# Optimization experiments

Hardware: AMD Instinct MI355X
Metric: run time of the kernel (lower is better)

The kernel has to match this reference:

```python
import jax, jax.numpy as jnp
import numpy as np

IN_DIM = 256
QK_DIM = IN_DIM // 8


def setup_inputs() -> dict:
    key = jax.random.key(0)
    ks = jax.random.split(key, 10)
    B, C, W, H = 4, IN_DIM, 64, 64
    a = jax.random.normal(ks[0], (B, C, W, H), dtype=jnp.float32)
    b = jax.random.normal(ks[1], (B, C, W, H), dtype=jnp.float32)
    c = jax.random.uniform(ks[2], (B, 1, 2 * W, 2 * H), dtype=jnp.float32)
    scale = 0.02
    wq = jax.random.normal(ks[3], (QK_DIM, C), dtype=jnp.float32) * scale
    bq = jnp.zeros((QK_DIM,), dtype=jnp.float32)
    wk = jax.random.normal(ks[4], (QK_DIM, C), dtype=jnp.float32) * scale
    bk = jnp.zeros((QK_DIM,), dtype=jnp.float32)
    wv = jax.random.normal(ks[5], (C, C), dtype=jnp.float32) * scale
    bv = jnp.zeros((C,), dtype=jnp.float32)
    gamma = jnp.ones((1,), dtype=jnp.float32)
    return {"a": a, "b": b, "c": c, "wq": wq, "bq": bq, "wk": wk,
            "bk": bk, "wv": wv, "bv": bv, "gamma": gamma}


def reference(a, b, c, wq, bq, wk, bk, wv, bv, gamma):
    B, C, W, H = a.shape
    N = W * H
    # F.interpolate(c, scale_factor=1/down_rate, mode='nearest'): output idx i -> input idx i*down_rate
    down = c.shape[2] // W
    cd = c[:, :, ::down, ::down]                      # [B,1,W,H]
    # 1x1 convs as channel contractions
    q = jnp.einsum('bchw,oc->bohw', a, wq) + bq[None, :, None, None]
    k = jnp.einsum('bchw,oc->bohw', b, wk) + bk[None, :, None, None]
    v = jnp.einsum('bchw,oc->bohw', a, wv) + bv[None, :, None, None]
    qf = q.reshape(B, QK_DIM, N)                      # proj_query^T rows are spatial
    kf = k.reshape(B, QK_DIM, N)
    vf = v.reshape(B, C, N)
    sim = jnp.einsum('bdi,bdj->bij', qf, kf)          # [B,N,N]
    cflat = cd.reshape(B, N)
    # mask[b,i,j] = cflat[b,i] (per-query multiplicative logit scaling)
    logits = sim * cflat[:, :, None]
    attn = jax.nn.softmax(logits, axis=-1)            # [B,N,N]
    out_attn = jnp.einsum('bcj,bij->bci', vf, attn).reshape(B, C, W, H)
    out = gamma * a * cd + (1.0 - cd) * out_attn
    return out
```

## Files before the change

### kernel.cpp

```cpp
#include <hip/hip_runtime.h>

#define LOG2E 1.44269504088896340736f

typedef __attribute__((ext_vector_type(8))) short short8;
typedef __attribute__((ext_vector_type(4))) float float4v;
typedef __attribute__((ext_vector_type(2))) float float2v;
typedef __attribute__((ext_vector_type(2))) int int2v;
typedef __attribute__((ext_vector_type(4))) int int4v;

__device__ inline unsigned short f2bf(float f) {
    union { float f; unsigned u; } v; v.f = f;
    unsigned r = v.u + 0x7fffu + ((v.u >> 16) & 1u);
    return (unsigned short)(r >> 16);
}
__device__ inline float bf2f(unsigned short u) {
    union { unsigned u; float f; } v; v.u = ((unsigned)u) << 16;
    return v.f;
}
__device__ inline unsigned pk_bf16(float a, float b) {
    union { float f; unsigned u; } ua, ub; ua.f = a; ub.f = b;
    return __builtin_amdgcn_perm(ub.u + 0x8000u, ua.u + 0x8000u, 0x07060302u);
}
__device__ inline unsigned cvtpk_bf16(float a, float b) {
    unsigned r;
    asm("v_cvt_pk_bf16_f32 %0, %1, %2" : "=v"(r) : "v"(a), "v"(b));
    return r;
}

__global__ void wcvt_kernel(const float* __restrict__ wq, const float* __restrict__ wk,
                            const float* __restrict__ wv, unsigned short* __restrict__ Wbf)
{
    int idx = blockIdx.x * 256 + threadIdx.x;
    int e4  = idx * 4;
    int row = e4 >> 8, col = e4 & 255;
    const float* src = (row < 32) ? (wq + row * 256 + col)
                     : (row < 64) ? (wk + (row - 32) * 256 + col)
                                  : (wv + (row - 64) * 256 + col);
    float4v v = *(const float4v*)src;
    int2v p;
    p.x = (unsigned)f2bf(v[0]) | ((unsigned)f2bf(v[1]) << 16);
    p.y = (unsigned)f2bf(v[2]) | ((unsigned)f2bf(v[3]) << 16);
    *(int2v*)(Wbf + e4) = p;
}

__launch_bounds__(512, 2)
__global__ void proj_kernel(const float* __restrict__ a_p, const float* __restrict__ b_p,
                            const float* __restrict__ c_p,
                            const float* __restrict__ bq, const float* __restrict__ bk,
                            const float* __restrict__ bv,
                            const unsigned short* __restrict__ Wbf,
                            unsigned short* __restrict__ Qg, unsigned short* __restrict__ Kg,
                            unsigned short* __restrict__ Vg)
{
    __shared__ __align__(16) unsigned short At[64 * 266];
    __shared__ __align__(16) unsigned short Bt[64 * 266];
    __shared__ float bias[320];
    __shared__ float cdl[64];

    const int t    = threadIdx.x;
    const int blk  = blockIdx.x;
    const int b    = blk & 3;
    const int tile = blk >> 2;
    const int i0   = tile * 64;
    const int lane = t & 63;
    const int w    = t >> 6;
    const int q    = lane >> 4;
    const int n    = lane & 15;
    const int it   = w & 3;
    const int mh   = w >> 2;

    {
        const int arr = t >> 8, tt = t & 255;
        unsigned* dst = (unsigned*)(arr ? Bt : At);
        const float* base = (arr ? b_p : a_p) + (size_t)b * 256 * 4096 + i0;
#pragma unroll
        for (int r = 0; r < 8; ++r) {
            int task = r * 256 + tt;
            int cp = task >> 4, px4 = (task & 15) * 4;
            const float* s0 = base + (size_t)(2 * cp) * 4096 + px4;
            float4v r0 = *(const float4v*)s0;
            float4v r1 = *(const float4v*)(s0 + 4096);
#pragma unroll
            for (int k = 0; k < 4; ++k)
                dst[(px4 + k) * 133 + cp] = pk_bf16(r0[k], r1[k]);
        }
        if (t < 320) bias[t] = (t < 32) ? bq[t] : (t < 64) ? bk[t - 32] : bv[t - 64];
        else if (t < 384) cdl[t - 320] = c_p[b * 16384 + tile * 256 + (t - 320) * 2];
    }
    __syncthreads();

    float4v acc[10];
#pragma unroll
    for (int j = 0; j < 10; ++j) acc[j] = (float4v){0.f, 0.f, 0.f, 0.f};

#pragma unroll 2
    for (int kc = 0; kc < 8; ++kc) {
        short8 xa = *(const short8*)&At[(it * 16 + n) * 266 + kc * 32 + q * 8];
        short8 xb = xa;
        if (mh == 0)
            xb = *(const short8*)&Bt[(it * 16 + n) * 266 + kc * 32 + q * 8];
#pragma unroll
        for (int j = 0; j < 10; ++j) {
            int mt = mh * 10 + j;
            short8 wf = *(const short8*)(Wbf + (size_t)(mt * 16 + n) * 256 + kc * 32 + q * 8);
            short8 bsel = (mt == 2 || mt == 3) ? xb : xa;
            acc[j] = __builtin_amdgcn_mfma_f32_16x16x32_bf16(wf, bsel, acc[j], 0, 0, 0);
        }
    }
    __syncthreads();

    unsigned short* QKst = At;
    unsigned short* Vst  = Bt;
    {
        const float cdq = cdl[it * 16 + n] * LOG2E;
#pragma unroll
        for (int j = 0; j < 10; ++j) {
            int mt = mh * 10 + j;
            float4v bv4 = *(const float4v*)&bias[mt * 16 + q * 4];
            float v0 = acc[j][0] + bv4[0], v1 = acc[j][1] + bv4[1];
            float v2 = acc[j][2] + bv4[2], v3 = acc[j][3] + bv4[3];
            if (mt < 2) {
                v0 *= cdq; v1 *= cdq; v2 *= cdq; v3 *= cdq;
                int2v pk; pk.x = (int)pk_bf16(v0, v1); pk.y = (int)pk_bf16(v2, v3);
                *(int2v*)&QKst[(it * 16 + n) * 72 + mt * 16 + q * 4] = pk;
            } else if (mt < 4) {
                int2v pk; pk.x = (int)pk_bf16(v0, v1); pk.y = (int)pk_bf16(v2, v3);
                *(int2v*)&QKst[(it * 16 + n) * 72 + mt * 16 + q * 4] = pk;
            } else {
                int p = ((n >> 2) * 8) + ((it & 1) * 4) + (n & 3);
                int cbase = mt * 16 - 64 + q * 4;
                int jb = it >> 1;
                Vst[((jb * 256) + cbase + 0) * 32 + p] = f2bf(v0);
                Vst[((jb * 256) + cbase + 1) * 32 + p] = f2bf(v1);
                Vst[((jb * 256) + cbase + 2) * 32 + p] = f2bf(v2);
                Vst[((jb * 256) + cbase + 3) * 32 + p] = f2bf(v3);
            }
        }
    }
    __syncthreads();

    {
        int i = t >> 3, h8 = t & 7;
        int4v v = *(const int4v*)&QKst[i * 72 + h8 * 8];
        unsigned short* dstp = (h8 < 4)
            ? Qg + (size_t)(b * 4096 + i0 + i) * 32 + h8 * 8
            : Kg + (size_t)(b * 4096 + i0 + i) * 32 + (h8 - 4) * 8;
        *(int4v*)dstp = v;
    }
    {
#pragma unroll
        for (int k = 0; k < 4; ++k) {
            int flat = k * 512 + t;
            int4v v = *(const int4v*)&Vst[flat * 8];
            int jb = flat >> 10;
            *(int4v*)(Vg + (size_t)(b * 128 + tile * 2 + jb) * 8192 + (flat & 1023) * 8) = v;
        }
    }
}

__launch_bounds__(256, 3)
__global__ void attn_kernel(const unsigned short* __restrict__ Qg,
                            const unsigned short* __restrict__ Kg,
                            const unsigned short* __restrict__ Vg,
                            unsigned short* __restrict__ Opart, float* __restrict__ lsum)
{
    const int t    = threadIdx.x;
    const int blk  = blockIdx.x;
    const int b    = blk & 3;
    const int rt   = (blk >> 2) & 63;
    const int s    = blk >> 8;
    const int ni   = (s == 2) ? 32 : 48;
    const int lidx = (s << 8) | (rt << 2) | b;
    const int i0   = rt * 64;
    const int lane = t & 63;
    const int w    = t >> 6;
    const int q    = lane >> 4;
    const int n    = lane & 15;

    short8 qf[4];
#pragma unroll
    for (int ig = 0; ig < 4; ++ig)
        qf[ig] = *(const short8*)(Qg + (size_t)(b * 4096 + i0 + ig * 16 + n) * 32 + q * 8);

    float4v acc[4][4];
#pragma unroll
    for (int ig = 0; ig < 4; ++ig)
#pragma unroll
        for (int ct = 0; ct < 4; ++ct) acc[ig][ct] = (float4v){0.f, 0.f, 0.f, 0.f};
    float lsc[4] = {0.f, 0.f, 0.f, 0.f};

    const float4v m16v = (float4v){-16.f, -16.f, -16.f, -16.f};

    const unsigned short* kb = Kg + (size_t)(b * 4096 + s * 1536 + n) * 32 + q * 8;
    const unsigned short* vb = Vg + ((size_t)((b * 128 + s * 48) * 256 + w * 64 + n)) * 32 + q * 8;

    short8 vf[4];
#pragma unroll
    for (int ct = 0; ct < 4; ++ct)
        vf[ct] = *(const short8*)(vb + ct * 512);
    short8 kf0 = *(const short8*)(kb);
    short8 kf1 = *(const short8*)(kb + 512);

    short8 pfc[4];
    {
        float4v s0[4], s1[4];
#pragma unroll
        for (int ig = 0; ig < 4; ++ig) {
            s0[ig] = __builtin_amdgcn_mfma_f32_16x16x32_bf16(kf0, qf[ig], m16v, 0, 0, 0);
            s1[ig] = __builtin_amdgcn_mfma_f32_16x16x32_bf16(kf1, qf[ig], m16v, 0, 0, 0);
        }
        kf0 = *(const short8*)(kb + 1024);
        kf1 = *(const short8*)(kb + 1536);
#pragma unroll
        for (int ig = 0; ig < 4; ++ig) {
            float p0 = __builtin_amdgcn_exp2f(s0[ig][0]), p1 = __builtin_amdgcn_exp2f(s0[ig][1]);
            float p2 = __builtin_amdgcn_exp2f(s0[ig][2]), p3 = __builtin_amdgcn_exp2f(s0[ig][3]);
            float p4 = __builtin_amdgcn_exp2f(s1[ig][0]), p5 = __builtin_amdgcn_exp2f(s1[ig][1]);
            float p6 = __builtin_amdgcn_exp2f(s1[ig][2]), p7 = __builtin_amdgcn_exp2f(s1[ig][3]);
            lsc[ig] += ((p0 + p1) + (p2 + p3)) + ((p4 + p5) + (p6 + p7));
            union { short8 s8; unsigned u[4]; } pf_;
            pf_.u[0] = cvtpk_bf16(p0, p1);
            pf_.u[1] = cvtpk_bf16(p2, p3);
            pf_.u[2] = cvtpk_bf16(p4, p5);
            pf_.u[3] = cvtpk_bf16(p6, p7);
            pfc[ig] = pf_.s8;
        }
    }
    kb += 2048;
    vb += 8192;

#pragma unroll 1
    for (int it = 0; it < ni - 1; ++it) {
        float4v s0[4], s1[4];
#pragma unroll
        for (int ig = 0; ig < 4; ++ig) {
            s0[ig] = __builtin_amdgcn_mfma_f32_16x16x32_bf16(kf0, qf[ig], m16v, 0, 0, 0);
            s1[ig] = __builtin_amdgcn_mfma_f32_16x16x32_bf16(kf1, qf[ig], m16v, 0, 0, 0);
        }
        kf0 = *(const short8*)(kb);
        kf1 = *(const short8*)(kb + 512);

        __builtin_amdgcn_s_setprio(1);
#pragma unroll
        for (int ig = 0; ig < 4; ++ig)
#pragma unroll
            for (int ct = 0; ct < 4; ++ct)
                acc[ig][ct] = __builtin_amdgcn_mfma_f32_16x16x32_bf16(pfc[ig], vf[ct], acc[ig][ct], 0, 0, 0);
        __builtin_amdgcn_s_setprio(0);

#pragma unroll
        for (int ct = 0; ct < 4; ++ct)
            vf[ct] = *(const short8*)(vb + ct * 512);

#pragma unroll
        for (int ig = 0; ig < 4; ++ig) {
            float p0 = __builtin_amdgcn_exp2f(s0[ig][0]), p1 = __builtin_amdgcn_exp2f(s0[ig][1]);
            float p2 = __builtin_amdgcn_exp2f(s0[ig][2]), p3 = __builtin_amdgcn_exp2f(s0[ig][3]);
            float p4 = __builtin_amdgcn_exp2f(s1[ig][0]), p5 = __builtin_amdgcn_exp2f(s1[ig][1]);
            float p6 = __builtin_amdgcn_exp2f(s1[ig][2]), p7 = __builtin_amdgcn_exp2f(s1[ig][3]);
            lsc[ig] += ((p0 + p1) + (p2 + p3)) + ((p4 + p5) + (p6 + p7));
            union { short8 s8; unsigned u[4]; } pf_;
            pf_.u[0] = cvtpk_bf16(p0, p1);
            pf_.u[1] = cvtpk_bf16(p2, p3);
            pf_.u[2] = cvtpk_bf16(p4, p5);
            pf_.u[3] = cvtpk_bf16(p6, p7);
            pfc[ig] = pf_.s8;
        }

        kb += 1024;
        vb += 8192;
    }

#pragma unroll
    for (int ig = 0; ig < 4; ++ig)
#pragma unroll
        for (int ct = 0; ct < 4; ++ct)
            acc[ig][ct] = __builtin_amdgcn_mfma_f32_16x16x32_bf16(pfc[ig], vf[ct], acc[ig][ct], 0, 0, 0);

    const size_t obase = (size_t)lidx * 16384;
#pragma unroll
    for (int ig = 0; ig < 4; ++ig)
#pragma unroll
        for (int ct = 0; ct < 4; ++ct) {
            int c = w * 64 + ct * 16 + n;
            int i = ig * 16 + q * 4;
            int2v pk;
            pk.x = (int)pk_bf16(acc[ig][ct][0], acc[ig][ct][1]);
            pk.y = (int)pk_bf16(acc[ig][ct][2], acc[ig][ct][3]);
            *(int2v*)(Opart + obase + (size_t)c * 64 + i) = pk;
        }
#pragma unroll
    for (int ig = 0; ig < 4; ++ig) {
        float v = lsc[ig];
        v += __shfl_xor(v, 16, 64);
        v += __shfl_xor(v, 32, 64);
        if (w == 0 && lane < 16)
            lsum[(size_t)lidx * 64 + ig * 16 + lane] = v;
    }
}

__launch_bounds__(256, 4)
__global__ void combine_kernel(const float* __restrict__ a_p, const float* __restrict__ c_p,
                               const float* __restrict__ gamma_p,
                               const unsigned short* __restrict__ Opart,
                               const float* __restrict__ lsum, float* __restrict__ out)
{
    __shared__ float invL[64];
    __shared__ float cdl[64];

    const int t   = threadIdx.x;
    const int blk = blockIdx.x;
    const int b   = blk & 3;
    const int rt  = (blk >> 2) & 63;
    const int cs  = blk >> 8;
    const int i0  = rt * 64;

    if (t < 64) {
        float L = 0.f;
#pragma unroll
        for (int s = 0; s < 3; ++s)
            L += lsum[(size_t)((s << 8) | (rt << 2) | b) * 64 + t];
        invL[t] = 1.0f / L;
        cdl[t] = c_p[b * 16384 + rt * 256 + 2 * t];
    }
    __syncthreads();

    const float gam = gamma_p[0];
    const int c  = cs * 32 + (t >> 3);
    const int e8 = (t & 7) * 8;
    float o[8];
#pragma unroll
    for (int r = 0; r < 8; ++r) o[r] = 0.f;
#pragma unroll
    for (int s = 0; s < 3; ++s) {
        int idx = (s << 8) | (rt << 2) | b;
        int4v pv = *(const int4v*)(Opart + (size_t)idx * 16384 + (size_t)c * 64 + e8);
#pragma unroll
        for (int h = 0; h < 4; ++h) {
            unsigned u = (unsigned)pv[h];
            o[2 * h]     += bf2f((unsigned short)(u & 0xffffu));
            o[2 * h + 1] += bf2f((unsigned short)(u >> 16));
        }
    }
    size_t gi = (size_t)(b * 256 + c) * 4096 + i0 + e8;
    float4v a0 = *(const float4v*)(a_p + gi);
    float4v a1 = *(const float4v*)(a_p + gi + 4);
    float4v ov0, ov1;
#pragma unroll
    for (int r = 0; r < 4; ++r) {
        float cd0 = cdl[e8 + r],     l0 = invL[e8 + r];
        float cd1 = cdl[e8 + 4 + r], l1 = invL[e8 + 4 + r];
        ov0[r] = gam * a0[r] * cd0 + (1.0f - cd0) * (o[r] * l0);
        ov1[r] = gam * a1[r] * cd1 + (1.0f - cd1) * (o[4 + r] * l1);
    }
    *(float4v*)(out + gi) = ov0;
    *(float4v*)(out + gi + 4) = ov1;
}

extern "C" void kernel_launch(void* const* d_in, const int* in_sizes, int n_in,
                              void* d_out, int out_size, void* d_ws, size_t ws_size,
                              hipStream_t stream)
{
    const float* a_p   = (const float*)d_in[0];
    const float* b_p   = (const float*)d_in[1];
    const float* c_p   = (const float*)d_in[2];
    const float* wq    = (const float*)d_in[3];
    const float* bq    = (const float*)d_in[4];
    const float* wk    = (const float*)d_in[5];
    const float* bk    = (const float*)d_in[6];
    const float* wv    = (const float*)d_in[7];
    const float* bv    = (const float*)d_in[8];
    const float* gamma = (const float*)d_in[9];
    float* out = (float*)d_out;

    unsigned short* Qg    = (unsigned short*)d_ws;
    unsigned short* Kg    = Qg + (size_t)4 * 4096 * 32;
    unsigned short* Vg    = Kg + (size_t)4 * 4096 * 32;
    unsigned short* Wbf   = Vg + (size_t)4 * 256 * 4096;
    unsigned short* Opart = Wbf + (size_t)320 * 256;
    float*          lsum  = (float*)(Opart + (size_t)768 * 16384);

    wcvt_kernel<<<80, 256, 0, stream>>>(wq, wk, wv, Wbf);
    proj_kernel<<<256, 512, 0, stream>>>(a_p, b_p, c_p, bq, bk, bv, Wbf, Qg, Kg, Vg);
    attn_kernel<<<768, 256, 0, stream>>>(Qg, Kg, Vg, Opart, lsum);
    combine_kernel<<<2048, 256, 0, stream>>>(a_p, c_p, gamma, Opart, lsum, out);
}
```

Before: 176.8 us.

## Split QK^T and exp across waves, share probabilities via LDS double buffer

Previously every wave computed scores and exponentials for all 64 query rows, so the QK^T MFMAs and exp2 work were repeated four times per block. Now each wave computes only its own 16-row group and writes the bf16 probabilities to a double-buffered shared-memory tile. After a barrier, all waves read the four groups back for the PV MFMAs. This removes the redundant score and exp work and frees registers, at the cost of a __syncthreads per iteration and extra LDS traffic.

```diff
diff --git a/kernel.cpp b/kernel.cpp
--- a/kernel.cpp
+++ b/kernel.cpp
@@ -164,6 +164,8 @@
                             const unsigned short* __restrict__ Vg,
                             unsigned short* __restrict__ Opart, float* __restrict__ lsum)
 {
+    __shared__ __align__(16) unsigned short Pbuf[2][4][64 * 8];
+
     const int t    = threadIdx.x;
     const int blk  = blockIdx.x;
     const int b    = blk & 3;
@@ -177,17 +179,14 @@
     const int q    = lane >> 4;
     const int n    = lane & 15;
 
-    short8 qf[4];
+    short8 qf = *(const short8*)(Qg + (size_t)(b * 4096 + i0 + w * 16 + n) * 32 + q * 8);
+
+    float4v acc[4][4];
 #pragma unroll
     for (int ig = 0; ig < 4; ++ig)
-        qf[ig] = *(const short8*)(Qg + (size_t)(b * 4096 + i0 + ig * 16 + n) * 32 + q * 8);
-
-    float4v acc[4][4];
-#pragma unroll
-    for (int ig = 0; ig < 4; ++ig)
 #pragma unroll
         for (int ct = 0; ct < 4; ++ct) acc[ig][ct] = (float4v){0.f, 0.f, 0.f, 0.f};
-    float lsc[4] = {0.f, 0.f, 0.f, 0.f};
+    float lsc = 0.f;
 
     const float4v m16v = (float4v){-16.f, -16.f, -16.f, -16.f};
 
@@ -201,71 +200,68 @@
     short8 kf0 = *(const short8*)(kb);
     short8 kf1 = *(const short8*)(kb + 512);
 
-    short8 pfc[4];
-    {
-        float4v s0[4], s1[4];
-#pragma unroll
-        for (int ig = 0; ig < 4; ++ig) {
-            s0[ig] = __builtin_amdgcn_mfma_f32_16x16x32_bf16(kf0, qf[ig], m16v, 0, 0, 0);
-            s1[ig] = __builtin_amdgcn_mfma_f32_16x16x32_bf16(kf1, qf[ig], m16v, 0, 0, 0);
-        }
+    {
+        float4v s0 = __builtin_amdgcn_mfma_f32_16x16x32_bf16(kf0, qf, m16v, 0, 0, 0);
+        float4v s1 = __builtin_amdgcn_mfma_f32_16x16x32_bf16(kf1, qf, m16v, 0, 0, 0);
         kf0 = *(const short8*)(kb + 1024);
         kf1 = *(const short8*)(kb + 1536);
-#pragma unroll
-        for (int ig = 0; ig < 4; ++ig) {
-            float p0 = __builtin_amdgcn_exp2f(s0[ig][0]), p1 = __builtin_amdgcn_exp2f(s0[ig][1]);
-            float p2 = __builtin_amdgcn_exp2f(s0[ig][2]), p3 = __builtin_amdgcn_exp2f(s0[ig][3]);
-            float p4 = __builtin_amdgcn_exp2f(s1[ig][0]), p5 = __builtin_amdgcn_exp2f(s1[ig][1]);
-            float p6 = __builtin_amdgcn_exp2f(s1[ig][2]), p7 = __builtin_amdgcn_exp2f(s1[ig][3]);
-            lsc[ig] += ((p0 + p1) + (p2 + p3)) + ((p4 + p5) + (p6 + p7));
+        float p0 = __builtin_amdgcn_exp2f(s0[0]), p1 = __builtin_amdgcn_exp2f(s0[1]);
+        float p2 = __builtin_amdgcn_exp2f(s0[2]), p3 = __builtin_amdgcn_exp2f(s0[3]);
+        float p4 = __builtin_amdgcn_exp2f(s1[0]), p5 = __builtin_amdgcn_exp2f(s1[1]);
+        float p6 = __builtin_amdgcn_exp2f(s1[2]), p7 = __builtin_amdgcn_exp2f(s1[3]);
+        lsc += ((p0 + p1) + (p2 + p3)) + ((p4 + p5) + (p6 + p7));
+        union { short8 s8; unsigned u[4]; } pf_;
+        pf_.u[0] = cvtpk_bf16(p0, p1);
+        pf_.u[1] = cvtpk_bf16(p2, p3);
+        pf_.u[2] = cvtpk_bf16(p4, p5);
+        pf_.u[3] = cvtpk_bf16(p6, p7);
+        *(short8*)&Pbuf[0][w][lane * 8] = pf_.s8;
+    }
+    __syncthreads();
+    short8 pfc[4];
+#pragma unroll
+    for (int ig = 0; ig < 4; ++ig)
+        pfc[ig] = *(const short8*)&Pbuf[0][ig][lane * 8];
+
+    kb += 2048;
+    vb += 8192;
+
+#pragma unroll 1
+    for (int it = 0; it < ni - 1; ++it) {
+        float4v s0 = __builtin_amdgcn_mfma_f32_16x16x32_bf16(kf0, qf, m16v, 0, 0, 0);
+        float4v s1 = __builtin_amdgcn_mfma_f32_16x16x32_bf16(kf1, qf, m16v, 0, 0, 0);
+        kf0 = *(const short8*)(kb);
+        kf1 = *(const short8*)(kb + 512);
+
+        __builtin_amdgcn_s_setprio(1);
+#pragma unroll
+        for (int ig = 0; ig < 4; ++ig)
+#pragma unroll
+            for (int ct = 0; ct < 4; ++ct)
+                acc[ig][ct] = __builtin_amdgcn_mfma_f32_16x16x32_bf16(pfc[ig], vf[ct], acc[ig][ct], 0, 0, 0);
+        __builtin_amdgcn_s_setprio(0);
+
+#pragma unroll
+        for (int ct = 0; ct < 4; ++ct)
+            vf[ct] = *(const short8*)(vb + ct * 512);
+
+        {
+            float p0 = __builtin_amdgcn_exp2f(s0[0]), p1 = __builtin_amdgcn_exp2f(s0[1]);
+            float p2 = __builtin_amdgcn_exp2f(s0[2]), p3 = __builtin_amdgcn_exp2f(s0[3]);
+            float p4 = __builtin_amdgcn_exp2f(s1[0]), p5 = __builtin_amdgcn_exp2f(s1[1]);
+            float p6 = __builtin_amdgcn_exp2f(s1[2]), p7 = __builtin_amdgcn_exp2f(s1[3]);
+            lsc += ((p0 + p1) + (p2 + p3)) + ((p4 + p5) + (p6 + p7));
             union { short8 s8; unsigned u[4]; } pf_;
             pf_.u[0] = cvtpk_bf16(p0, p1);
             pf_.u[1] = cvtpk_bf16(p2, p3);
             pf_.u[2] = cvtpk_bf16(p4, p5);
             pf_.u[3] = cvtpk_bf16(p6, p7);
-            pfc[ig] = pf_.s8;
-        }
-    }
-    kb += 2048;
-    vb += 8192;
-
-#pragma unroll 1
-    for (int it = 0; it < ni - 1; ++it) {
-        float4v s0[4], s1[4];
-#pragma unroll
-        for (int ig = 0; ig < 4; ++ig) {
-            s0[ig] = __builtin_amdgcn_mfma_f32_16x16x32_bf16(kf0, qf[ig], m16v, 0, 0, 0);
-            s1[ig] = __builtin_amdgcn_mfma_f32_16x16x32_bf16(kf1, qf[ig], m16v, 0, 0, 0);
-        }
-        kf0 = *(const short8*)(kb);
-        kf1 = *(const short8*)(kb + 512);
-
-        __builtin_amdgcn_s_setprio(1);
+            *(short8*)&Pbuf[(it + 1) & 1][w][lane * 8] = pf_.s8;
+        }
+        __syncthreads();
 #pragma unroll
         for (int ig = 0; ig < 4; ++ig)
-#pragma unroll
-            for (int ct = 0; ct < 4; ++ct)
-                acc[ig][ct] = __builtin_amdgcn_mfma_f32_16x16x32_bf16(pfc[ig], vf[ct], acc[ig][ct], 0, 0, 0);
-        __builtin_amdgcn_s_setprio(0);
-
-#pragma unroll
-        for (int ct = 0; ct < 4; ++ct)
-            vf[ct] = *(const short8*)(vb + ct * 512);
-
-#pragma unroll
-        for (int ig = 0; ig < 4; ++ig) {
-            float p0 = __builtin_amdgcn_exp2f(s0[ig][0]), p1 = __builtin_amdgcn_exp2f(s0[ig][1]);
-            float p2 = __builtin_amdgcn_exp2f(s0[ig][2]), p3 = __builtin_amdgcn_exp2f(s0[ig][3]);
-            float p4 = __builtin_amdgcn_exp2f(s1[ig][0]), p5 = __builtin_amdgcn_exp2f(s1[ig][1]);
-            float p6 = __builtin_amdgcn_exp2f(s1[ig][2]), p7 = __builtin_amdgcn_exp2f(s1[ig][3]);
-            lsc[ig] += ((p0 + p1) + (p2 + p3)) + ((p4 + p5) + (p6 + p7));
-            union { short8 s8; unsigned u[4]; } pf_;
-            pf_.u[0] = cvtpk_bf16(p0, p1);
-            pf_.u[1] = cvtpk_bf16(p2, p3);
-            pf_.u[2] = cvtpk_bf16(p4, p5);
-            pf_.u[3] = cvtpk_bf16(p6, p7);
-            pfc[ig] = pf_.s8;
-        }
+            pfc[ig] = *(const short8*)&Pbuf[(it + 1) & 1][ig][lane * 8];
 
         kb += 1024;
         vb += 8192;
@@ -289,13 +285,12 @@
             pk.y = (int)pk_bf16(acc[ig][ct][2], acc[ig][ct][3]);
             *(int2v*)(Opart + obase + (size_t)c * 64 + i) = pk;
         }
-#pragma unroll
-    for (int ig = 0; ig < 4; ++ig) {
-        float v = lsc[ig];
+    {
+        float v = lsc;
         v += __shfl_xor(v, 16, 64);
         v += __shfl_xor(v, 32, 64);
-        if (w == 0 && lane < 16)
-            lsum[(size_t)lidx * 64 + ig * 16 + lane] = v;
+        if (lane < 16)
+            lsum[(size_t)lidx * 64 + w * 16 + lane] = v;
     }
 }
 
```

New measurement: 175.3 us (median of 2 runs). About the same (-0.9%).
